# Kernel tuning notes

Hardware: AMD Instinct MI355X
Metric: run time of the kernel (lower is better)

Reference implementation:

```python
import jax, jax.numpy as jnp
import numpy as np


def setup_inputs() -> dict:
    key = jax.random.key(0)
    ks = jax.random.split(key, 8)
    B, N, C = 8, 4096, 128
    x = jax.random.normal(ks[0], (B, N, C), dtype=jnp.float32)
    spatial_pos = jax.random.randint(ks[1], (1, N, N), 0, 6, dtype=jnp.int32)
    sc = 1.0 / np.sqrt(C)
    W1 = jax.random.normal(ks[2], (C, C), dtype=jnp.float32) * sc
    b1 = jax.random.normal(ks[3], (C,), dtype=jnp.float32) * 0.01
    W2 = jax.random.normal(ks[4], (C, C // 8), dtype=jnp.float32) * sc
    b2 = jax.random.normal(ks[5], (C // 8,), dtype=jnp.float32) * 0.01
    Wb = jax.random.normal(ks[6], (C + C // 8, C), dtype=jnp.float32) * (1.0 / np.sqrt(C + C // 8))
    bb = jax.random.normal(ks[7], (C,), dtype=jnp.float32) * 0.01
    return {"x": x, "spatial_pos": spatial_pos, "W1": W1, "b1": b1,
            "W2": W2, "b2": b2, "Wb": Wb, "bb": bb}


def reference(x, spatial_pos, W1, b1, W2, b2, Wb, bb):
    # s=1, l=2: scale k=1 uses mask (spatial_pos <= 1), k=2 uses (spatial_pos == 2)
    sp = spatial_pos[0]                      # [N, N], batch-invariant
    m1 = (sp <= 1).astype(x.dtype)           # [N, N]
    m2 = (sp == 2).astype(x.dtype)           # [N, N]
    h1 = x @ W1 + b1                         # [B, N, C]
    h2 = x @ W2 + b2                         # [B, N, C//8]
    # torch.bmm(mask.expand(B,-1,-1), h) == einsum over shared mask
    f1 = jnp.einsum('ij,bjc->bic', m1, h1)   # [B, N, C]
    f2 = jnp.einsum('ij,bjc->bic', m2, h2)   # [B, N, C//8]
    feats = jnp.concatenate([f1, f2], axis=-1)  # [B, N, C + C//8]
    return feats @ Wb + bb                   # [B, N, output_dim]
```

## Files before the change

### kernel.cpp

```cpp
#include <hip/hip_runtime.h>
#include <stdint.h>

typedef unsigned short u16;
typedef __attribute__((ext_vector_type(8))) short short8;
typedef __attribute__((ext_vector_type(4))) float f32x4;

#define MFMA __builtin_amdgcn_mfma_f32_16x16x32_bf16

__device__ __forceinline__ u16 f2bf(float f) {
  union { float f; uint32_t u; } v; v.f = f;
  return (u16)((v.u + 0x7FFFu + ((v.u >> 16) & 1u)) >> 16);
}

#define GLOAD16(gp, lp) \
  __builtin_amdgcn_global_load_lds((const __attribute__((address_space(1))) uint32_t*)(gp), \
                                   (__attribute__((address_space(3))) uint32_t*)(lp), 16, 0, 0)

#define WS_H    0
#define WS_Q1   9502720
#define WS_Q2   9503232
#define WS_M1P  9503744
#define WS_M2P  11600896
#define WS_RS1  13698048
#define WS_RS2  13714432
#define WS_WSB  13730816

__global__ __launch_bounds__(256) void k0(const int* __restrict__ sp,
                                          unsigned long long* __restrict__ m1p,
                                          unsigned long long* __restrict__ m2p,
                                          float* __restrict__ rs1, float* __restrict__ rs2,
                                          const float* __restrict__ W1, const float* __restrict__ Wb,
                                          const float* __restrict__ b1, const float* __restrict__ b2,
                                          const float* __restrict__ W2,
                                          float* __restrict__ q1, float* __restrict__ q2,
                                          u16* __restrict__ wsbg) {
  const int tid = threadIdx.x;
  if (blockIdx.x < 1024) {
    int wave = tid >> 6, lane = tid & 63;
    int i = blockIdx.x * 4 + wave;
    const int* rowp = sp + (size_t)i * 4096;
    int c1 = 0, c2 = 0;
    for (int w = 0; w < 64; ++w) {
      int v = rowp[w * 64 + lane];
      unsigned long long bb1 = __ballot(v <= 1);
      unsigned long long bb2 = __ballot(v == 2);
      if (lane == 0) {
        m1p[(size_t)w * 4096 + i] = bb1;
        m2p[(size_t)w * 4096 + i] = bb2;
        c1 += __popcll(bb1);
        c2 += __popcll(bb2);
      }
    }
    if (lane == 0) { rs1[i] = (float)c1; rs2[i] = (float)c2; }
    return;
  }
  int idx = (int)(blockIdx.x - 1024) * 256 + tid;
  int a = idx >> 7, c = idx & 127;
  float acc = 0.f;
  for (int k = 0; k < 128; ++k) acc += W1[a * 128 + k] * Wb[k * 128 + c];
  wsbg[(((a >> 3) * 144) + c) * 8 + (a & 7)] = f2bf(acc);
  if (idx < 2048) {
    int k = idx >> 4, nn2 = idx & 15;
    wsbg[(((k >> 3) * 144) + 128 + nn2) * 8 + (k & 7)] = f2bf(W2[k * 16 + nn2]);
  }
  if (idx < 128) {
    float s1 = 0.f, s2 = 0.f;
    for (int k = 0; k < 128; ++k) s1 += b1[k] * Wb[k * 128 + idx];
    for (int k = 0; k < 16; ++k)  s2 += b2[k] * Wb[(128 + k) * 128 + idx];
    q1[idx] = s1; q2[idx] = s2;
  }
}

__global__ __launch_bounds__(256, 2) void kproj(const float* __restrict__ x,
                                                const u16* __restrict__ wsbg,
                                                u16* __restrict__ H) {
  __shared__ u16 wsb[18432];
  __shared__ u16 xs[64 * 136];
  __shared__ u16 hs[64 * 146];
  const int tid = threadIdx.x;
  const int bid = blockIdx.x;
  const int b = bid >> 6;
  const int kt = bid & 63;
  const size_t r0 = (size_t)b * 4096 + (size_t)kt * 64;

#pragma unroll
  for (int i = 0; i < 9; ++i)
    GLOAD16(wsbg + (i * 256 + tid) * 8, (char*)&wsb[0] + (i * 256 + tid) * 16);
  {
    const float* xp = x + (r0 + (tid >> 2)) * 128 + (tid & 3) * 32;
    u16* xd = xs + (tid >> 2) * 136 + (tid & 3) * 32;
#pragma unroll
    for (int i = 0; i < 4; ++i) {
      f32x4 a = ((const f32x4*)xp)[i * 2];
      f32x4 bq = ((const f32x4*)xp)[i * 2 + 1];
      short8 pk;
      pk[0] = (short)f2bf(a[0]); pk[1] = (short)f2bf(a[1]);
      pk[2] = (short)f2bf(a[2]); pk[3] = (short)f2bf(a[3]);
      pk[4] = (short)f2bf(bq[0]); pk[5] = (short)f2bf(bq[1]);
      pk[6] = (short)f2bf(bq[2]); pk[7] = (short)f2bf(bq[3]);
      *(short8*)(xd + i * 8) = pk;
    }
  }
  __syncthreads();

  const int w = tid >> 6, l = tid & 63, lr = l & 15, lg = l >> 4;
  f32x4 acc[9];
  f32x4 zz = {0.f, 0.f, 0.f, 0.f};
#pragma unroll
  for (int fn = 0; fn < 9; ++fn) acc[fn] = zz;
#pragma unroll
  for (int kf = 0; kf < 4; ++kf) {
    short8 af = *(const short8*)(xs + (w * 16 + lr) * 136 + kf * 32 + lg * 8);
#pragma unroll
    for (int fn = 0; fn < 9; ++fn) {
      short8 bf = *(const short8*)(wsb + (((kf * 4 + lg) * 144) + fn * 16 + lr) * 8);
      acc[fn] = MFMA(af, bf, acc[fn], 0, 0, 0);
    }
  }
  __syncthreads();
#pragma unroll
  for (int fn = 0; fn < 9; ++fn)
#pragma unroll
    for (int g = 0; g < 4; ++g)
      hs[(w * 16 + lg * 4 + g) * 146 + fn * 16 + lr] = f2bf(acc[fn][g]);
  __syncthreads();
  for (int i = 0; i < 5; ++i) {
    int e = i * 256 + tid;
    if (e < 1152) {
      int jbl = e / 144, n = e % 144;
      union { u16 s[8]; uint4 v; } pk;
#pragma unroll
      for (int r = 0; r < 8; ++r) pk.s[r] = hs[(jbl * 8 + r) * 146 + n];
      int kf = jbl >> 2, lgw = jbl & 3, fn = n >> 4, lrw = n & 15;
      size_t di = ((((size_t)kt * 2 + kf) * 8 + b) * 9 + fn) * 512 + (lgw * 16 + lrw) * 8;
      *(uint4*)(H + di) = pk.v;
    }
  }
}

__device__ __forceinline__ short8 expand_byte(uint32_t wd, int lgsh) {
  uint32_t b = (wd >> lgsh) & 0xFFu;
  uint32_t t = b * 0x8001u;
  union { uint32_t u[4]; short8 s; } r;
  r.u[0] = (t & 0x00010001u) * 0x3F80u;
  r.u[1] = (t & 0x00040004u) * 0x0FE0u;
  r.u[2] = (t & 0x00100010u) * 0x03F8u;
  r.u[3] = (t & 0x00400040u) * 0x00FEu;
  return r.s;
}

__global__ __launch_bounds__(512, 2) void kb1(const u16* __restrict__ H,
                                              const char* __restrict__ M1b,
                                              const char* __restrict__ M2b,
                                              const float* __restrict__ rs1, const float* __restrict__ rs2,
                                              const float* __restrict__ q1, const float* __restrict__ q2,
                                              const float* __restrict__ Wb, const float* __restrict__ bb,
                                              float* __restrict__ out) {
  __shared__ u16 bt[3][9216];
  __shared__ u16 mkb[3][1024];
  __shared__ u16 f2s[128 * 40];
  __shared__ u16 wb2s[4096];

  const int tid = threadIdx.x;
  const int bid = blockIdx.x;
  const int b = bid & 7;
  const int i0 = (bid >> 3) * 128;

  const int w = tid >> 6, l = tid & 63, lr = l & 15, lg = l >> 4;
  const int h = w >> 2, c = w & 3;
  const int lgsh = lg * 8;

  const u16* pB0 = H + b * 4608 + (size_t)tid * 8;
  const u16* pB1 = H + ((512 + tid) < 576 ? (b * 4608 + (size_t)(512 + tid) * 8)
                                          : (36864 + b * 4608 + (size_t)(512 + tid - 576) * 8));
  const u16* pB2 = H + 36864 + b * 4608 + (size_t)(448 + tid) * 8;
  const int mc = tid - 128;
  const char* pM = ((mc & 64) ? M2b : M1b) + (size_t)i0 * 8 + (size_t)(mc & 63) * 16;
  const int dB0 = tid * 16, dB1 = (512 + tid) * 16, dB2 = (1024 + tid) * 16;
  const int dM = ((mc >> 6) & 1) * 1024 + (mc & 63) * 16;

#define STAGE(BUF) { \
    GLOAD16(pB0, (char*)&bt[BUF][0] + dB0); \
    GLOAD16(pB1, (char*)&bt[BUF][0] + dB1); \
    if (tid < 128) GLOAD16(pB2, (char*)&bt[BUF][0] + dB2); \
    else if (tid < 256) GLOAD16(pM, (char*)&mkb[BUF][0] + dM); \
    pB0 += 73728; pB1 += 73728; pB2 += 73728; pM += 32768; }

  const int f00 = (c * 2 + 0) * 512 + l * 8;
  const int f01 = (c * 2 + 1) * 512 + l * 8;
  const int f10 = 4608 + f00;
  const int f11 = 4608 + f01;
  const int fm0 = 4096 + l * 8;
  const int fm1 = 4608 + 4096 + l * 8;

  f32x4 zz = {0.f, 0.f, 0.f, 0.f};
  f32x4 a00 = zz, a01 = zz, a10 = zz, a11 = zz, a20 = zz, a21 = zz, a30 = zz, a31 = zz;
  f32x4 acc2 = zz;

#define WAITV { if (w < 4) asm volatile("s_waitcnt vmcnt(3)" ::: "memory"); \
                else asm volatile("s_waitcnt vmcnt(2)" ::: "memory"); }

#define COMPUTE(BUF) { \
    const u16* src_ = &bt[BUF][0]; \
    const char* mk_ = (const char*)&mkb[BUF][0]; \
    uint2 c0_ = *(const uint2*)(mk_ + ((4 * h + 0) * 16 + lr) * 8); \
    uint2 c1_ = *(const uint2*)(mk_ + ((4 * h + 1) * 16 + lr) * 8); \
    uint2 c2_ = *(const uint2*)(mk_ + ((4 * h + 2) * 16 + lr) * 8); \
    uint2 c3_ = *(const uint2*)(mk_ + ((4 * h + 3) * 16 + lr) * 8); \
    uint2 cm_ = *(const uint2*)(mk_ + 1024 + (w * 16 + lr) * 8); \
    short8 b00_ = *(const short8*)(src_ + f00); \
    short8 b01_ = *(const short8*)(src_ + f01); \
    short8 b10_ = *(const short8*)(src_ + f10); \
    short8 b11_ = *(const short8*)(src_ + f11); \
    short8 bm0_ = *(const short8*)(src_ + fm0); \
    short8 bm1_ = *(const short8*)(src_ + fm1); \
    short8 e0x_ = expand_byte(c0_.x, lgsh), e0y_ = expand_byte(c0_.y, lgsh); \
    short8 e1x_ = expand_byte(c1_.x, lgsh), e1y_ = expand_byte(c1_.y, lgsh); \
    short8 e2x_ = expand_byte(c2_.x, lgsh), e2y_ = expand_byte(c2_.y, lgsh); \
    short8 e3x_ = expand_byte(c3_.x, lgsh), e3y_ = expand_byte(c3_.y, lgsh); \
    short8 emx_ = expand_byte(cm_.x, lgsh), emy_ = expand_byte(cm_.y, lgsh); \
    __builtin_amdgcn_s_setprio(1); \
    a00 = MFMA(e0x_, b00_, a00, 0, 0, 0); \
    a01 = MFMA(e0x_, b01_, a01, 0, 0, 0); \
    a00 = MFMA(e0y_, b10_, a00, 0, 0, 0); \
    a01 = MFMA(e0y_, b11_, a01, 0, 0, 0); \
    a10 = MFMA(e1x_, b00_, a10, 0, 0, 0); \
    a11 = MFMA(e1x_, b01_, a11, 0, 0, 0); \
    a10 = MFMA(e1y_, b10_, a10, 0, 0, 0); \
    a11 = MFMA(e1y_, b11_, a11, 0, 0, 0); \
    a20 = MFMA(e2x_, b00_, a20, 0, 0, 0); \
    a21 = MFMA(e2x_, b01_, a21, 0, 0, 0); \
    a20 = MFMA(e2y_, b10_, a20, 0, 0, 0); \
    a21 = MFMA(e2y_, b11_, a21, 0, 0, 0); \
    a30 = MFMA(e3x_, b00_, a30, 0, 0, 0); \
    a31 = MFMA(e3x_, b01_, a31, 0, 0, 0); \
    a30 = MFMA(e3y_, b10_, a30, 0, 0, 0); \
    a31 = MFMA(e3y_, b11_, a31, 0, 0, 0); \
    acc2 = MFMA(emx_, bm0_, acc2, 0, 0, 0); \
    acc2 = MFMA(emy_, bm1_, acc2, 0, 0, 0); \
    __builtin_amdgcn_s_setprio(0); }

#define PHASE(BUF, BUF2) { WAITV; __builtin_amdgcn_s_barrier(); STAGE(BUF2); COMPUTE(BUF) }

  STAGE(0);
  STAGE(1);

#pragma unroll
  for (int i = 0; i < 8; ++i) {
    int e = i * 512 + tid;
    int r_ = e & 7, nn = (e >> 3) & 127, jb = e >> 10;
    int k = jb * 8 + r_;
    wb2s[e] = f2bf((k < 16) ? Wb[(128 + k) * 128 + nn] : 0.f);
  }

  for (int it = 0; it < 20; ++it) {
    PHASE(0, 2);
    PHASE(1, 0);
    PHASE(2, 1);
  }
  PHASE(0, 2);
  PHASE(1, 0);
  { WAITV; __builtin_amdgcn_s_barrier(); COMPUTE(2) }
  { asm volatile("s_waitcnt vmcnt(0)" ::: "memory");
    __builtin_amdgcn_s_barrier(); COMPUTE(0) }

#pragma unroll
  for (int j = 0; j < 4; ++j) {
    int e = tid * 4 + j;
    f2s[(e >> 4) * 40 + 16 + (e & 15)] = 0;
  }
#pragma unroll
  for (int gg = 0; gg < 4; ++gg)
    f2s[(w * 16 + lg * 4 + gg) * 40 + lr] = f2bf(acc2[gg]);
  __syncthreads();

  short8 bw0 = *(const short8*)(wb2s + ((lg * 128) + (c * 2 + 0) * 16 + lr) * 8);
  short8 bw1 = *(const short8*)(wb2s + ((lg * 128) + (c * 2 + 1) * 16 + lr) * 8);
  {
    short8 af0 = *(const short8*)(f2s + ((4 * h + 0) * 16 + lr) * 40 + lg * 8);
    short8 af1 = *(const short8*)(f2s + ((4 * h + 1) * 16 + lr) * 40 + lg * 8);
    short8 af2 = *(const short8*)(f2s + ((4 * h + 2) * 16 + lr) * 40 + lg * 8);
    short8 af3 = *(const short8*)(f2s + ((4 * h + 3) * 16 + lr) * 40 + lg * 8);
    a00 = MFMA(af0, bw0, a00, 0, 0, 0);
    a01 = MFMA(af0, bw1, a01, 0, 0, 0);
    a10 = MFMA(af1, bw0, a10, 0, 0, 0);
    a11 = MFMA(af1, bw1, a11, 0, 0, 0);
    a20 = MFMA(af2, bw0, a20, 0, 0, 0);
    a21 = MFMA(af2, bw1, a21, 0, 0, 0);
    a30 = MFMA(af3, bw0, a30, 0, 0, 0);
    a31 = MFMA(af3, bw1, a31, 0, 0, 0);
  }

  const int col0 = (c * 2 + 0) * 16 + lr, col1 = (c * 2 + 1) * 16 + lr;
  const float q10 = q1[col0], q20 = q2[col0], bb0 = bb[col0];
  const float q11 = q1[col1], q21 = q2[col1], bb1 = bb[col1];
#pragma unroll
  for (int i = 0; i < 4; ++i) {
    f32x4 v0 = (i == 0) ? a00 : (i == 1) ? a10 : (i == 2) ? a20 : a30;
    f32x4 v1 = (i == 0) ? a01 : (i == 1) ? a11 : (i == 2) ? a21 : a31;
#pragma unroll
    for (int gg = 0; gg < 4; ++gg) {
      int row = (4 * h + i) * 16 + lg * 4 + gg;
      float r1 = rs1[i0 + row], r2 = rs2[i0 + row];
      size_t obase = ((size_t)b * 4096 + i0 + row) * 128;
      out[obase + col0] = v0[gg] + r1 * q10 + r2 * q20 + bb0;
      out[obase + col1] = v1[gg] + r1 * q11 + r2 * q21 + bb1;
    }
  }
}

extern "C" void kernel_launch(void* const* d_in, const int* in_sizes, int n_in,
                              void* d_out, int out_size, void* d_ws, size_t ws_size,
                              hipStream_t stream) {
  const float* x  = (const float*)d_in[0];
  const int*   sp = (const int*)d_in[1];
  const float* W1 = (const float*)d_in[2];
  const float* b1 = (const float*)d_in[3];
  const float* W2 = (const float*)d_in[4];
  const float* b2 = (const float*)d_in[5];
  const float* Wb = (const float*)d_in[6];
  const float* bb = (const float*)d_in[7];
  float* out = (float*)d_out;
  char* ws = (char*)d_ws;

  u16* H = (u16*)(ws + WS_H);
  float* q1 = (float*)(ws + WS_Q1);
  float* q2 = (float*)(ws + WS_Q2);
  unsigned long long* m1p = (unsigned long long*)(ws + WS_M1P);
  unsigned long long* m2p = (unsigned long long*)(ws + WS_M2P);
  float* rs1 = (float*)(ws + WS_RS1);
  float* rs2 = (float*)(ws + WS_RS2);
  u16* wsbg = (u16*)(ws + WS_WSB);

  k0<<<1088, 256, 0, stream>>>(sp, m1p, m2p, rs1, rs2, W1, Wb, b1, b2, W2, q1, q2, wsbg);
  kproj<<<512, 256, 0, stream>>>(x, wsbg, H);
  kb1<<<256, 512, 0, stream>>>(H, (const char*)m1p, (const char*)m2p,
                               rs1, rs2, q1, q2, Wb, bb, out);
}
```

Measured before the change: 97.95 us.

## Switch main mask-GEMM to 32x32x16 MFMA with matching H layout

The main masked aggregation GEMM moves from 16x16x32 bf16 MFMA tiles to 32x32x16 tiles. Each wave now owns a 32x64 output block instead of 64x32. The H producer kernel, the staging layout, the mask byte expansion and the final Wb projection and epilogue are all re-indexed to match. This cuts the number of MFMA issues, LDS fragment reads and mask expansions per K step, and lowers LDS use for wb2s. The cost is larger per-instruction accumulators and a different register footprint under launch_bounds(512,2).

```diff
diff --git a/kernel.cpp b/kernel.cpp
--- a/kernel.cpp
+++ b/kernel.cpp
@@ -4,8 +4,10 @@
 typedef unsigned short u16;
 typedef __attribute__((ext_vector_type(8))) short short8;
 typedef __attribute__((ext_vector_type(4))) float f32x4;
+typedef __attribute__((ext_vector_type(16))) float f32x16;
 
 #define MFMA __builtin_amdgcn_mfma_f32_16x16x32_bf16
+#define MFMA32 __builtin_amdgcn_mfma_f32_32x32x16_bf16
 
 __device__ __forceinline__ u16 f2bf(float f) {
   union { float f; uint32_t u; } v; v.f = f;
@@ -124,22 +126,35 @@
     for (int g = 0; g < 4; ++g)
       hs[(w * 16 + lg * 4 + g) * 146 + fn * 16 + lr] = f2bf(acc[fn][g]);
   __syncthreads();
+  const size_t base = (size_t)kt * 73728 + (size_t)b * 9216;
   for (int i = 0; i < 5; ++i) {
-    int e = i * 256 + tid;
-    if (e < 1152) {
-      int jbl = e / 144, n = e % 144;
+    int ch = i * 256 + tid;
+    if (ch < 1152) {
       union { u16 s[8]; uint4 v; } pk;
-#pragma unroll
-      for (int r = 0; r < 8; ++r) pk.s[r] = hs[(jbl * 8 + r) * 146 + n];
-      int kf = jbl >> 2, lgw = jbl & 3, fn = n >> 4, lrw = n & 15;
-      size_t di = ((((size_t)kt * 2 + kf) * 8 + b) * 9 + fn) * 512 + (lgw * 16 + lrw) * 8;
+      size_t di;
+      if (ch < 1024) {
+        int cb = ch >> 8, ks = (ch >> 6) & 3, ll = ch & 63;
+        int row = ks * 16 + (ll >> 5) * 8;
+        int col = cb * 32 + (ll & 31);
+#pragma unroll
+        for (int e = 0; e < 8; ++e) pk.s[e] = hs[(row + e) * 146 + col];
+        di = base + (size_t)((cb * 4 + ks) * 512 + ll * 8);
+      } else {
+        int c2 = ch - 1024;
+        int kf = c2 >> 6, ll = c2 & 63;
+        int row = kf * 32 + (ll >> 4) * 8;
+        int col = 128 + (ll & 15);
+#pragma unroll
+        for (int e = 0; e < 8; ++e) pk.s[e] = hs[(row + e) * 146 + col];
+        di = base + (size_t)(8192 + kf * 512 + ll * 8);
+      }
       *(uint4*)(H + di) = pk.v;
     }
   }
 }
 
-__device__ __forceinline__ short8 expand_byte(uint32_t wd, int lgsh) {
-  uint32_t b = (wd >> lgsh) & 0xFFu;
+__device__ __forceinline__ short8 expand_byte(uint32_t wd, int sh) {
+  uint32_t b = (wd >> sh) & 0xFFu;
   uint32_t t = b * 0x8001u;
   union { uint32_t u[4]; short8 s; } r;
   r.u[0] = (t & 0x00010001u) * 0x3F80u;
@@ -159,7 +174,7 @@
   __shared__ u16 bt[3][9216];
   __shared__ u16 mkb[3][1024];
   __shared__ u16 f2s[128 * 40];
-  __shared__ u16 wb2s[4096];
+  __shared__ u16 wb2s[2048];
 
   const int tid = threadIdx.x;
   const int bid = blockIdx.x;
@@ -167,13 +182,14 @@
   const int i0 = (bid >> 3) * 128;
 
   const int w = tid >> 6, l = tid & 63, lr = l & 15, lg = l >> 4;
-  const int h = w >> 2, c = w & 3;
+  const int h = w >> 1, c2 = w & 1;
+  const int cb0 = c2 * 2, cb1 = c2 * 2 + 1;
+  const int sh32 = (l >> 5) * 8;
   const int lgsh = lg * 8;
 
-  const u16* pB0 = H + b * 4608 + (size_t)tid * 8;
-  const u16* pB1 = H + ((512 + tid) < 576 ? (b * 4608 + (size_t)(512 + tid) * 8)
-                                          : (36864 + b * 4608 + (size_t)(512 + tid - 576) * 8));
-  const u16* pB2 = H + 36864 + b * 4608 + (size_t)(448 + tid) * 8;
+  const u16* pB0 = H + (size_t)b * 9216 + (size_t)tid * 8;
+  const u16* pB1 = H + (size_t)b * 9216 + (size_t)(512 + tid) * 8;
+  const u16* pB2 = H + (size_t)b * 9216 + (size_t)(1024 + tid) * 8;
   const int mc = tid - 128;
   const char* pM = ((mc & 64) ? M2b : M1b) + (size_t)i0 * 8 + (size_t)(mc & 63) * 16;
   const int dB0 = tid * 16, dB1 = (512 + tid) * 16, dB2 = (1024 + tid) * 16;
@@ -186,16 +202,16 @@
     else if (tid < 256) GLOAD16(pM, (char*)&mkb[BUF][0] + dM); \
     pB0 += 73728; pB1 += 73728; pB2 += 73728; pM += 32768; }
 
-  const int f00 = (c * 2 + 0) * 512 + l * 8;
-  const int f01 = (c * 2 + 1) * 512 + l * 8;
-  const int f10 = 4608 + f00;
-  const int f11 = 4608 + f01;
-  const int fm0 = 4096 + l * 8;
-  const int fm1 = 4608 + 4096 + l * 8;
-
-  f32x4 zz = {0.f, 0.f, 0.f, 0.f};
-  f32x4 a00 = zz, a01 = zz, a10 = zz, a11 = zz, a20 = zz, a21 = zz, a30 = zz, a31 = zz;
-  f32x4 acc2 = zz;
+  const int fb0 = (cb0 * 4) * 512 + l * 8;
+  const int fb1 = (cb1 * 4) * 512 + l * 8;
+  const int fm0 = 8192 + l * 8;
+  const int fm1 = 8192 + 512 + l * 8;
+
+  f32x16 am0, am1;
+  f32x4 acc2;
+#pragma unroll
+  for (int i = 0; i < 16; ++i) { am0[i] = 0.f; am1[i] = 0.f; }
+  acc2[0] = acc2[1] = acc2[2] = acc2[3] = 0.f;
 
 #define WAITV { if (w < 4) asm volatile("s_waitcnt vmcnt(3)" ::: "memory"); \
                 else asm volatile("s_waitcnt vmcnt(2)" ::: "memory"); }
@@ -203,41 +219,35 @@
 #define COMPUTE(BUF) { \
     const u16* src_ = &bt[BUF][0]; \
     const char* mk_ = (const char*)&mkb[BUF][0]; \
-    uint2 c0_ = *(const uint2*)(mk_ + ((4 * h + 0) * 16 + lr) * 8); \
-    uint2 c1_ = *(const uint2*)(mk_ + ((4 * h + 1) * 16 + lr) * 8); \
-    uint2 c2_ = *(const uint2*)(mk_ + ((4 * h + 2) * 16 + lr) * 8); \
-    uint2 c3_ = *(const uint2*)(mk_ + ((4 * h + 3) * 16 + lr) * 8); \
+    uint2 c1_ = *(const uint2*)(mk_ + (h * 32 + (l & 31)) * 8); \
     uint2 cm_ = *(const uint2*)(mk_ + 1024 + (w * 16 + lr) * 8); \
-    short8 b00_ = *(const short8*)(src_ + f00); \
-    short8 b01_ = *(const short8*)(src_ + f01); \
-    short8 b10_ = *(const short8*)(src_ + f10); \
-    short8 b11_ = *(const short8*)(src_ + f11); \
+    short8 bA0_ = *(const short8*)(src_ + fb0); \
+    short8 bA1_ = *(const short8*)(src_ + fb0 + 512); \
+    short8 bA2_ = *(const short8*)(src_ + fb0 + 1024); \
+    short8 bA3_ = *(const short8*)(src_ + fb0 + 1536); \
+    short8 bB0_ = *(const short8*)(src_ + fb1); \
+    short8 bB1_ = *(const short8*)(src_ + fb1 + 512); \
+    short8 bB2_ = *(const short8*)(src_ + fb1 + 1024); \
+    short8 bB3_ = *(const short8*)(src_ + fb1 + 1536); \
     short8 bm0_ = *(const short8*)(src_ + fm0); \
     short8 bm1_ = *(const short8*)(src_ + fm1); \
-    short8 e0x_ = expand_byte(c0_.x, lgsh), e0y_ = expand_byte(c0_.y, lgsh); \
-    short8 e1x_ = expand_byte(c1_.x, lgsh), e1y_ = expand_byte(c1_.y, lgsh); \
-    short8 e2x_ = expand_byte(c2_.x, lgsh), e2y_ = expand_byte(c2_.y, lgsh); \
-    short8 e3x_ = expand_byte(c3_.x, lgsh), e3y_ = expand_byte(c3_.y, lgsh); \
-    short8 emx_ = expand_byte(cm_.x, lgsh), emy_ = expand_byte(cm_.y, lgsh); \
+    short8 e0_ = expand_byte(c1_.x, sh32); \
+    short8 e1_ = expand_byte(c1_.x, sh32 + 16); \
+    short8 e2_ = expand_byte(c1_.y, sh32); \
+    short8 e3_ = expand_byte(c1_.y, sh32 + 16); \
+    short8 em0_ = expand_byte(cm_.x, lgsh); \
+    short8 em1_ = expand_byte(cm_.y, lgsh); \
     __builtin_amdgcn_s_setprio(1); \
-    a00 = MFMA(e0x_, b00_, a00, 0, 0, 0); \
-    a01 = MFMA(e0x_, b01_, a01, 0, 0, 0); \
-    a00 = MFMA(e0y_, b10_, a00, 0, 0, 0); \
-    a01 = MFMA(e0y_, b11_, a01, 0, 0, 0); \
-    a10 = MFMA(e1x_, b00_, a10, 0, 0, 0); \
-    a11 = MFMA(e1x_, b01_, a11, 0, 0, 0); \
-    a10 = MFMA(e1y_, b10_, a10, 0, 0, 0); \
-    a11 = MFMA(e1y_, b11_, a11, 0, 0, 0); \
-    a20 = MFMA(e2x_, b00_, a20, 0, 0, 0); \
-    a21 = MFMA(e2x_, b01_, a21, 0, 0, 0); \
-    a20 = MFMA(e2y_, b10_, a20, 0, 0, 0); \
-    a21 = MFMA(e2y_, b11_, a21, 0, 0, 0); \
-    a30 = MFMA(e3x_, b00_, a30, 0, 0, 0); \
-    a31 = MFMA(e3x_, b01_, a31, 0, 0, 0); \
-    a30 = MFMA(e3y_, b10_, a30, 0, 0, 0); \
-    a31 = MFMA(e3y_, b11_, a31, 0, 0, 0); \
-    acc2 = MFMA(emx_, bm0_, acc2, 0, 0, 0); \
-    acc2 = MFMA(emy_, bm1_, acc2, 0, 0, 0); \
+    am0 = MFMA32(e0_, bA0_, am0, 0, 0, 0); \
+    am1 = MFMA32(e0_, bB0_, am1, 0, 0, 0); \
+    am0 = MFMA32(e1_, bA1_, am0, 0, 0, 0); \
+    am1 = MFMA32(e1_, bB1_, am1, 0, 0, 0); \
+    am0 = MFMA32(e2_, bA2_, am0, 0, 0, 0); \
+    am1 = MFMA32(e2_, bB2_, am1, 0, 0, 0); \
+    am0 = MFMA32(e3_, bA3_, am0, 0, 0, 0); \
+    am1 = MFMA32(e3_, bB3_, am1, 0, 0, 0); \
+    acc2 = MFMA(em0_, bm0_, acc2, 0, 0, 0); \
+    acc2 = MFMA(em1_, bm1_, acc2, 0, 0, 0); \
     __builtin_amdgcn_s_setprio(0); }
 
 #define PHASE(BUF, BUF2) { WAITV; __builtin_amdgcn_s_barrier(); STAGE(BUF2); COMPUTE(BUF) }
@@ -246,11 +256,10 @@
   STAGE(1);
 
 #pragma unroll
-  for (int i = 0; i < 8; ++i) {
+  for (int i = 0; i < 4; ++i) {
     int e = i * 512 + tid;
-    int r_ = e & 7, nn = (e >> 3) & 127, jb = e >> 10;
-    int k = jb * 8 + r_;
-    wb2s[e] = f2bf((k < 16) ? Wb[(128 + k) * 128 + nn] : 0.f);
+    int cb = e >> 9, rem = e & 511, ll = rem >> 3, ee = rem & 7;
+    wb2s[e] = f2bf(Wb[(128 + (ll >> 5) * 8 + ee) * 128 + cb * 32 + (ll & 31)]);
   }
 
   for (int it = 0; it < 20; ++it) {
@@ -265,47 +274,28 @@
     __builtin_amdgcn_s_barrier(); COMPUTE(0) }
 
 #pragma unroll
-  for (int j = 0; j < 4; ++j) {
-    int e = tid * 4 + j;
-    f2s[(e >> 4) * 40 + 16 + (e & 15)] = 0;
-  }
-#pragma unroll
   for (int gg = 0; gg < 4; ++gg)
     f2s[(w * 16 + lg * 4 + gg) * 40 + lr] = f2bf(acc2[gg]);
   __syncthreads();
 
-  short8 bw0 = *(const short8*)(wb2s + ((lg * 128) + (c * 2 + 0) * 16 + lr) * 8);
-  short8 bw1 = *(const short8*)(wb2s + ((lg * 128) + (c * 2 + 1) * 16 + lr) * 8);
   {
-    short8 af0 = *(const short8*)(f2s + ((4 * h + 0) * 16 + lr) * 40 + lg * 8);
-    short8 af1 = *(const short8*)(f2s + ((4 * h + 1) * 16 + lr) * 40 + lg * 8);
-    short8 af2 = *(const short8*)(f2s + ((4 * h + 2) * 16 + lr) * 40 + lg * 8);
-    short8 af3 = *(const short8*)(f2s + ((4 * h + 3) * 16 + lr) * 40 + lg * 8);
-    a00 = MFMA(af0, bw0, a00, 0, 0, 0);
-    a01 = MFMA(af0, bw1, a01, 0, 0, 0);
-    a10 = MFMA(af1, bw0, a10, 0, 0, 0);
-    a11 = MFMA(af1, bw1, a11, 0, 0, 0);
-    a20 = MFMA(af2, bw0, a20, 0, 0, 0);
-    a21 = MFMA(af2, bw1, a21, 0, 0, 0);
-    a30 = MFMA(af3, bw0, a30, 0, 0, 0);
-    a31 = MFMA(af3, bw1, a31, 0, 0, 0);
-  }
-
-  const int col0 = (c * 2 + 0) * 16 + lr, col1 = (c * 2 + 1) * 16 + lr;
+    short8 af = *(const short8*)(f2s + (h * 32 + (l & 31)) * 40 + (l >> 5) * 8);
+    short8 bw0 = *(const short8*)(wb2s + cb0 * 512 + l * 8);
+    short8 bw1 = *(const short8*)(wb2s + cb1 * 512 + l * 8);
+    am0 = MFMA32(af, bw0, am0, 0, 0, 0);
+    am1 = MFMA32(af, bw1, am1, 0, 0, 0);
+  }
+
+  const int col0 = cb0 * 32 + (l & 31), col1 = cb1 * 32 + (l & 31);
   const float q10 = q1[col0], q20 = q2[col0], bb0 = bb[col0];
   const float q11 = q1[col1], q21 = q2[col1], bb1 = bb[col1];
 #pragma unroll
-  for (int i = 0; i < 4; ++i) {
-    f32x4 v0 = (i == 0) ? a00 : (i == 1) ? a10 : (i == 2) ? a20 : a30;
-    f32x4 v1 = (i == 0) ? a01 : (i == 1) ? a11 : (i == 2) ? a21 : a31;
-#pragma unroll
-    for (int gg = 0; gg < 4; ++gg) {
-      int row = (4 * h + i) * 16 + lg * 4 + gg;
-      float r1 = rs1[i0 + row], r2 = rs2[i0 + row];
-      size_t obase = ((size_t)b * 4096 + i0 + row) * 128;
-      out[obase + col0] = v0[gg] + r1 * q10 + r2 * q20 + bb0;
-      out[obase + col1] = v1[gg] + r1 * q11 + r2 * q21 + bb1;
-    }
+  for (int r = 0; r < 16; ++r) {
+    int row = h * 32 + (r & 3) + 8 * (r >> 2) + 4 * (l >> 5);
+    float r1 = rs1[i0 + row], r2 = rs2[i0 + row];
+    size_t obase = ((size_t)b * 4096 + i0 + row) * 128;
+    out[obase + col0] = am0[r] + r1 * q10 + r2 * q20 + bb0;
+    out[obase + col1] = am1[r] + r1 * q11 + r2 * q21 + bb1;
   }
 }
 
```

New measurement: 89.24 us. 8.9% less time.
